# Kernel optimization log

Hardware: AMD Instinct MI355X
Metric: run time of the kernel (lower is better)

Reference implementation:

```python
import jax, jax.numpy as jnp
import numpy as np

B, L, H, IN, NL = 8, 32768, 96, 1, 2


def _init(k, shape):
    # PyTorch LSTM/Linear default: U(-1/sqrt(H), 1/sqrt(H))
    return jax.random.uniform(k, shape, jnp.float32, -1.0, 1.0) / np.float32(np.sqrt(H))


def setup_inputs() -> dict:
    key = jax.random.key(0)
    ks = jax.random.split(key, 16)
    W_ih_0 = _init(ks[0], (4 * H, IN))
    W_hh_0 = _init(ks[1], (4 * H, H))
    b_ih_0 = _init(ks[2], (4 * H,))
    b_hh_0 = _init(ks[3], (4 * H,))
    W_ih_1 = _init(ks[4], (4 * H, H))
    W_hh_1 = _init(ks[5], (4 * H, H))
    b_ih_1 = _init(ks[6], (4 * H,))
    b_hh_1 = _init(ks[7], (4 * H,))
    # custom _L.reset_parameters: input-gate bias -=2, forget-gate bias +=2 on BOTH biases
    off = jnp.concatenate([jnp.full((H,), -2.0), jnp.full((H,), 2.0), jnp.zeros((2 * H,))]).astype(jnp.float32)
    b_0 = b_ih_0 + b_hh_0 + 2.0 * off  # combined bias per layer (they only ever add)
    b_1 = b_ih_1 + b_hh_1 + 2.0 * off
    head_w = _init(ks[8], (1, H))
    head_b = _init(ks[9], (1,))
    h0 = jnp.zeros((NL, H), jnp.float32)  # nn.Parameter initial hidden
    c0 = jnp.zeros((NL, H), jnp.float32)  # nn.Parameter initial cell
    x = 0.5 * jax.random.normal(ks[10], (B, L), jnp.float32)
    return {"x": x, "W_ih_0": W_ih_0, "W_hh_0": W_hh_0, "b_0": b_0,
            "W_ih_1": W_ih_1, "W_hh_1": W_hh_1, "b_1": b_1,
            "h0": h0, "c0": c0, "head_w": head_w, "head_b": head_b}


def _lstm_layer(x, W_ih, W_hh, b, h0, c0):
    # x: (B, L, D_in) -> hidden outputs (B, L, H). PyTorch gate order: i, f, g, o.
    Bn = x.shape[0]
    Hd = W_hh.shape[1]
    xp = jnp.einsum('bld,gd->blg', x, W_ih) + b  # (B, L, 4H), precompute input proj

    def step(carry, xt):
        h, c = carry
        gates = xt + h @ W_hh.T
        i, f, g, o = jnp.split(gates, 4, axis=-1)
        c = jax.nn.sigmoid(f) * c + jax.nn.sigmoid(i) * jnp.tanh(g)
        h = jax.nn.sigmoid(o) * jnp.tanh(c)
        return (h, c), h

    h0b = jnp.broadcast_to(h0, (Bn, Hd))
    c0b = jnp.broadcast_to(c0, (Bn, Hd))
    _, hs = jax.lax.scan(step, (h0b, c0b), jnp.swapaxes(xp, 0, 1))  # (L, B, H)
    return jnp.swapaxes(hs, 0, 1)


def reference(x, W_ih_0, W_hh_0, b_0, W_ih_1, W_hh_1, b_1, h0, c0, head_w, head_b):
    feats = x[:, :, None]  # (B, L, 1)
    feats = _lstm_layer(feats, W_ih_0, W_hh_0, b_0, h0[0], c0[0])
    feats = _lstm_layer(feats, W_ih_1, W_hh_1, b_1, h0[1], c0[1])
    # head: Linear(H, 1) then squeeze last dim -> (B, L)
    return jnp.einsum('blh,oh->bl', feats, head_w) + head_b[0]
```

## Files before the change

### kernel.cpp

```cpp
#include <hip/hip_runtime.h>

#define HDIM 96
#define G4   384
#define LSEQ 32768
#define BATCH 8
#define TCH   1024
#define NCH   (LSEQ / TCH)

#define L2E  1.4426950408889634f
#define SNEG (-L2E)
#define SPOS (2.0f * L2E)

__device__ __forceinline__ float tanh_(float x) {
    return fmaf(-2.f, __builtin_amdgcn_rcpf(1.f + __builtin_amdgcn_exp2f(SPOS * x)), 1.f);
}

#define DPPSTEP(v, CTRL) { \
    int t_ = __builtin_amdgcn_update_dpp(0, __float_as_int(v), CTRL, 0xF, 0xF, true); \
    v += __int_as_float(t_); }
#define DPPADDV(u, v, CTRL) { \
    int t_ = __builtin_amdgcn_update_dpp(0, __float_as_int(v), CTRL, 0xF, 0xF, true); \
    u += __int_as_float(t_); }

#define QBCAST(DST, SRCI, CTRL) \
    float DST = __int_as_float(__builtin_amdgcn_update_dpp(0, (SRCI), (CTRL), 0xF, 0xF, true));

#define BARL() asm volatile("s_waitcnt lgkmcnt(0)\n\ts_barrier" ::: "memory")

#define PIN4x3(A,B,C) asm volatile("" : \
  "+v"(A.x),"+v"(A.y),"+v"(A.z),"+v"(A.w), \
  "+v"(B.x),"+v"(B.y),"+v"(B.z),"+v"(B.w), \
  "+v"(C.x),"+v"(C.y),"+v"(C.z),"+v"(C.w));

#define SC4(V, S) { V.x *= (S); V.y *= (S); V.z *= (S); V.w *= (S); }

#define WLOADPIN(W) \
    const float4* pI = reinterpret_cast<const float4*>((W) + (size_t)e        * HDIM + 12*s); \
    const float4* pF = reinterpret_cast<const float4*>((W) + (size_t)(96 + e) * HDIM + 12*s); \
    const float4* pG = reinterpret_cast<const float4*>((W) + (size_t)(192+ e) * HDIM + 12*s); \
    const float4* pO = reinterpret_cast<const float4*>((W) + (size_t)(288+ e) * HDIM + 12*s); \
    float4 wI0=pI[0], wI1=pI[1], wI2=pI[2]; \
    float4 wF0=pF[0], wF1=pF[1], wF2=pF[2]; \
    float4 wG0=pG[0], wG1=pG[1], wG2=pG[2]; \
    float4 wO0=pO[0], wO1=pO[1], wO2=pO[2]; \
    SC4(wI0,SNEG) SC4(wI1,SNEG) SC4(wI2,SNEG) \
    SC4(wF0,SNEG) SC4(wF1,SNEG) SC4(wF2,SNEG) \
    SC4(wG0,SPOS) SC4(wG1,SPOS) SC4(wG2,SPOS) \
    SC4(wO0,SNEG) SC4(wO1,SNEG) SC4(wO2,SNEG) \
    PIN4x3(wI0,wI1,wI2) PIN4x3(wF0,wF1,wF2) PIN4x3(wG0,wG1,wG2) PIN4x3(wO0,wO1,wO2)

#define MVK(n, hv) \
  gi=fmaf(wI##n.x,hv.x,gi); gi=fmaf(wI##n.y,hv.y,gi); gi=fmaf(wI##n.z,hv.z,gi); gi=fmaf(wI##n.w,hv.w,gi); \
  gf=fmaf(wF##n.x,hv.x,gf); gf=fmaf(wF##n.y,hv.y,gf); gf=fmaf(wF##n.z,hv.z,gf); gf=fmaf(wF##n.w,hv.w,gf); \
  gg=fmaf(wG##n.x,hv.x,gg); gg=fmaf(wG##n.y,hv.y,gg); gg=fmaf(wG##n.z,hv.z,gg); gg=fmaf(wG##n.w,hv.w,gg); \
  go=fmaf(wO##n.x,hv.x,go); go=fmaf(wO##n.y,hv.y,go); go=fmaf(wO##n.z,hv.z,go); go=fmaf(wO##n.w,hv.w,go);

#define GATES_TAIL(DEST_STORE) \
    float uA = (tsel & 1) ? gf : gi,  vA = (tsel & 1) ? gi : gf; \
    float uB = (tsel & 1) ? go : gg,  vB = (tsel & 1) ? gg : go; \
    DPPADDV(uA, vA, 0xB1)  DPPADDV(uB, vB, 0xB1) \
    float uC = (tsel & 2) ? uB : uA,  vC = (tsel & 2) ? uA : uB; \
    DPPADDV(uC, vC, 0x4E) \
    DPPSTEP(uC, 0x141) \
    float E_ = __builtin_amdgcn_exp2f(uC); \
    float r_ = __builtin_amdgcn_rcpf(1.f + E_); \
    int ai = __float_as_int(fmaf(mC, r_, aC)); \
    QBCAST(si, ai, 0x00) \
    QBCAST(sf, ai, 0x55) \
    QBCAST(tg, ai, 0xAA) \
    QBCAST(so, ai, 0xFF) \
    cU = fmaf(sf, cU, si * tg); \
    float hN = so * tanh_(cU); \
    DEST_STORE

#define STEP0(RO, XT) { \
    const float4* hp = reinterpret_cast<const float4*>(hs + (RO) + 12 * s); \
    float4 hv0 = hp[0], hv1 = hp[1], hv2 = hp[2]; \
    float gi = fmaf(wiI, (XT), bbI); \
    float gf = fmaf(wiF, (XT), bbF); \
    float gg = fmaf(wiG, (XT), bbG); \
    float go = fmaf(wiO, (XT), bbO); \
    MVK(0, hv0) MVK(1, hv1) MVK(2, hv2) \
    GATES_TAIL( \
      if (w0l) { hs[((RO) ^ HDIM) + e] = hN; *hobp = hN; } \
      hobp += HDIM; ) }

#define STEP2(RO, XPV) { \
    const float4* hp = reinterpret_cast<const float4*>(hs + (RO) + 12 * s); \
    float4 hv0 = hp[0], hv1 = hp[1], hv2 = hp[2]; \
    float gi = (XPV).x, gf = (XPV).y, gg = (XPV).z, go = (XPV).w; \
    MVK(0, hv0) MVK(1, hv1) MVK(2, hv2) \
    GATES_TAIL( \
      if (w0l) { hs[((RO) ^ HDIM) + e] = hN; *h1p = hN; } \
      h1p += HDIM; ) }

#define WAIT_GE(PTR, VAL) \
    while (__hip_atomic_load((PTR), __ATOMIC_ACQUIRE, __HIP_MEMORY_SCOPE_AGENT) < (VAL)) \
        __builtin_amdgcn_s_sleep(2);

#define SIGNAL(PTR, VAL) \
    __hip_atomic_store((PTR), (VAL), __ATOMIC_RELEASE, __HIP_MEMORY_SCOPE_AGENT);

__global__ void init_flags(int* flags) {
    if (threadIdx.x < 64) flags[threadIdx.x] = 0;
}

__global__ void __launch_bounds__(768)
__attribute__((amdgpu_waves_per_eu(3, 3)))
lstm_pipe(const float* __restrict__ x,
          const float* __restrict__ Wih0, const float* __restrict__ Whh0, const float* __restrict__ b0v,
          const float* __restrict__ Wih1, const float* __restrict__ Whh1, const float* __restrict__ b1v,
          const float* __restrict__ h0v,  const float* __restrict__ c0v,
          const float* __restrict__ headw,const float* __restrict__ headb,
          float* __restrict__ h0buf, float* __restrict__ xpbuf, float* __restrict__ h1buf,
          int* flags, float* __restrict__ out)
{
    const int tid  = threadIdx.x;
    const int lane = tid & 63;
    const int e    = tid >> 3;
    const int s    = tid & 7;
    const bool w0l = ((lane & 7) == 0);

    int* flag0 = flags;
    int* flag1 = flags + 8;
    int* flag2 = flags + 16;
    int* flag3 = flags + 24;

    __shared__ __align__(16) float hs[2 * HDIM];
    __shared__ __align__(16) float h_sh[32 * HDIM];
    __shared__ float ph_sh[2 * G4];

    const int role = blockIdx.x >> 3;
    const int bidx = blockIdx.x & 7;

    const int tsel = (s & 3) ^ ((s & 4) ? 3 : 0);
    const float mC = (tsel == 2) ? -2.f : 1.f;
    const float aC = (tsel == 2) ?  1.f : 0.f;

    if (role == 0) {
        WLOADPIN(Whh0)
        const float wiI = Wih0[e]      * (SNEG * 0.125f);
        const float wiF = Wih0[96 + e] * (SNEG * 0.125f);
        const float wiG = Wih0[192+ e] * (SPOS * 0.125f);
        const float wiO = Wih0[288+ e] * (SNEG * 0.125f);
        const float bbI = b0v[e]       * (SNEG * 0.125f);
        const float bbF = b0v[96 + e]  * (SNEG * 0.125f);
        const float bbG = b0v[192+ e]  * (SPOS * 0.125f);
        const float bbO = b0v[288+ e]  * (SNEG * 0.125f);

        float cU = c0v[e];
        if (w0l) hs[e] = h0v[e];
        __syncthreads();

        const float* xb  = x + (size_t)bidx * LSEQ;
        float*       hobp = h0buf + (size_t)bidx * LSEQ * HDIM + e;

        float4 xA = *reinterpret_cast<const float4*>(xb);

#pragma unroll 1
        for (int gI = 0; gI < LSEQ / 8; ++gI) {
            float4 xB = *reinterpret_cast<const float4*>(xb + gI * 8 + 4);
            STEP0(0,    xA.x) BARL();
            STEP0(HDIM, xA.y) BARL();
            STEP0(0,    xA.z) BARL();
            STEP0(HDIM, xA.w) BARL();
            float4 xAn = *reinterpret_cast<const float4*>(
                xb + (((gI + 1) * 8 < LSEQ) ? (gI + 1) * 8 : LSEQ - 8));
            STEP0(0,    xB.x) BARL();
            STEP0(HDIM, xB.y) BARL();
            STEP0(0,    xB.z) BARL();
            STEP0(HDIM, xB.w)
            xA = xAn;
            if (((gI + 1) & 127) == 0) {
                __threadfence();
                __syncthreads();
                if (tid == 0) SIGNAL(&flag0[bidx], (gI + 1) >> 7)
            } else {
                BARL();
            }
        }
    } else if (role == 1) {
        const bool halfx = (tid >= G4);
        const int  g     = halfx ? tid - G4 : tid;
        const int  dstoff = (g % 96) * 4 + (g / 96);
        const float gsc  = (((g / 96) == 2) ? SPOS : SNEG) * 0.125f;
        const float4* Wxp = reinterpret_cast<const float4*>(Wih1 + (size_t)g * HDIM + (halfx ? 48 : 0));
        const float xbias = halfx ? 0.f : b1v[g] * gsc;

        float4 q0=Wxp[0],q1=Wxp[1],q2=Wxp[2],q3=Wxp[3],q4=Wxp[4],q5=Wxp[5],
               q6=Wxp[6],q7=Wxp[7],q8=Wxp[8],q9=Wxp[9],q10=Wxp[10],q11=Wxp[11];
        SC4(q0,gsc) SC4(q1,gsc) SC4(q2,gsc)  SC4(q3,gsc) SC4(q4,gsc)  SC4(q5,gsc)
        SC4(q6,gsc) SC4(q7,gsc) SC4(q8,gsc)  SC4(q9,gsc) SC4(q10,gsc) SC4(q11,gsc)
        PIN4x3(q0,q1,q2) PIN4x3(q3,q4,q5) PIN4x3(q6,q7,q8) PIN4x3(q9,q10,q11)

        const float* hsrcB = h0buf + (size_t)bidx * LSEQ * HDIM;

#pragma unroll 1
        for (int k = 0; k < NCH; ++k) {
            if (tid == 0) {
                WAIT_GE(&flag0[bidx], k + 1)
                if (k >= 2) WAIT_GE(&flag2[bidx], k - 1)
            }
            __syncthreads();
            __threadfence();

            const float* hsrc = hsrcB + (size_t)k * TCH * HDIM;
            float* xpd = xpbuf + ((size_t)bidx * 2 + (k & 1)) * TCH * G4;

#pragma unroll 1
            for (int t0 = 0; t0 < TCH; t0 += 32) {
                reinterpret_cast<float4*>(h_sh)[tid] =
                    reinterpret_cast<const float4*>(hsrc + (size_t)t0 * HDIM)[tid];
                BARL();
#pragma unroll 1
                for (int tt = 0; tt < 32; ++tt) {
                    const float4* h4 = reinterpret_cast<const float4*>(
                        h_sh + tt * HDIM + (halfx ? 48 : 0));
                    float a0 = xbias, a1 = 0.f, a2 = 0.f, a3 = 0.f;
                    float4 hv;
                    hv=h4[0];  a0=fmaf(q0.x, hv.x,a0); a1=fmaf(q0.y, hv.y,a1); a2=fmaf(q0.z, hv.z,a2); a3=fmaf(q0.w, hv.w,a3);
                    hv=h4[1];  a0=fmaf(q1.x, hv.x,a0); a1=fmaf(q1.y, hv.y,a1); a2=fmaf(q1.z, hv.z,a2); a3=fmaf(q1.w, hv.w,a3);
                    hv=h4[2];  a0=fmaf(q2.x, hv.x,a0); a1=fmaf(q2.y, hv.y,a1); a2=fmaf(q2.z, hv.z,a2); a3=fmaf(q2.w, hv.w,a3);
                    hv=h4[3];  a0=fmaf(q3.x, hv.x,a0); a1=fmaf(q3.y, hv.y,a1); a2=fmaf(q3.z, hv.z,a2); a3=fmaf(q3.w, hv.w,a3);
                    hv=h4[4];  a0=fmaf(q4.x, hv.x,a0); a1=fmaf(q4.y, hv.y,a1); a2=fmaf(q4.z, hv.z,a2); a3=fmaf(q4.w, hv.w,a3);
                    hv=h4[5];  a0=fmaf(q5.x, hv.x,a0); a1=fmaf(q5.y, hv.y,a1); a2=fmaf(q5.z, hv.z,a2); a3=fmaf(q5.w, hv.w,a3);
                    hv=h4[6];  a0=fmaf(q6.x, hv.x,a0); a1=fmaf(q6.y, hv.y,a1); a2=fmaf(q6.z, hv.z,a2); a3=fmaf(q6.w, hv.w,a3);
                    hv=h4[7];  a0=fmaf(q7.x, hv.x,a0); a1=fmaf(q7.y, hv.y,a1); a2=fmaf(q7.z, hv.z,a2); a3=fmaf(q7.w, hv.w,a3);
                    hv=h4[8];  a0=fmaf(q8.x, hv.x,a0); a1=fmaf(q8.y, hv.y,a1); a2=fmaf(q8.z, hv.z,a2); a3=fmaf(q8.w, hv.w,a3);
                    hv=h4[9];  a0=fmaf(q9.x, hv.x,a0); a1=fmaf(q9.y, hv.y,a1); a2=fmaf(q9.z, hv.z,a2); a3=fmaf(q9.w, hv.w,a3);
                    hv=h4[10]; a0=fmaf(q10.x,hv.x,a0); a1=fmaf(q10.y,hv.y,a1); a2=fmaf(q10.z,hv.z,a2); a3=fmaf(q10.w,hv.w,a3);
                    hv=h4[11]; a0=fmaf(q11.x,hv.x,a0); a1=fmaf(q11.y,hv.y,a1); a2=fmaf(q11.z,hv.z,a2); a3=fmaf(q11.w,hv.w,a3);
                    float part = (a0 + a1) + (a2 + a3);
                    float* ph2 = ph_sh + ((tt & 1) ? G4 : 0);
                    if (halfx) ph2[g] = part;
                    BARL();
                    if (!halfx) xpd[(size_t)(t0 + tt) * G4 + dstoff] = part + ph2[g];
                }
                BARL();
            }
            __threadfence();
            __syncthreads();
            if (tid == 0) SIGNAL(&flag1[bidx], k + 1)
        }
    } else if (role == 2) {
        WLOADPIN(Whh1)

        float cU = c0v[HDIM + e];
        if (w0l) hs[e] = h0v[HDIM + e];
        __syncthreads();

#pragma unroll 1
        for (int k = 0; k < NCH; ++k) {
            if (tid == 0) {
                WAIT_GE(&flag1[bidx], k + 1)
                if (k >= 2) WAIT_GE(&flag3[bidx], k - 1)
            }
            __syncthreads();
            __threadfence();

            const float4* xq  = reinterpret_cast<const float4*>(
                xpbuf + ((size_t)bidx * 2 + (k & 1)) * TCH * G4) + e;
            float* h1p = h1buf + ((size_t)bidx * 2 + (k & 1)) * TCH * HDIM + e;

            float4 a0 = xq[0], a1 = xq[HDIM], a2 = xq[2 * HDIM], a3 = xq[3 * HDIM];

#pragma unroll 1
            for (int gI = 0; gI < TCH / 8; ++gI) {
                const float4* xg = xq + (size_t)gI * 8 * HDIM;
                float4 b0_, b1_, b2_, b3_;
                STEP2(0,    a0) b0_ = xg[4 * HDIM]; BARL();
                STEP2(HDIM, a1) b1_ = xg[5 * HDIM]; BARL();
                STEP2(0,    a2) b2_ = xg[6 * HDIM]; BARL();
                STEP2(HDIM, a3) b3_ = xg[7 * HDIM]; BARL();
                const float4* xn = xq + (size_t)((gI + 1 < TCH / 8) ? (gI + 1) * 8 : TCH - 8) * HDIM;
                STEP2(0,    b0_) a0 = xn[0];        BARL();
                STEP2(HDIM, b1_) a1 = xn[HDIM];     BARL();
                STEP2(0,    b2_) a2 = xn[2 * HDIM]; BARL();
                STEP2(HDIM, b3_) a3 = xn[3 * HDIM]; BARL();
            }
            __threadfence();
            __syncthreads();
            if (tid == 0) SIGNAL(&flag2[bidx], k + 1)
        }
    } else {
        const float hb = headb[0];
        float4 wv[24];
#pragma unroll
        for (int j = 0; j < 24; ++j) wv[j] = reinterpret_cast<const float4*>(headw)[j];

#pragma unroll 1
        for (int k = 0; k < NCH; ++k) {
            if (tid == 0) WAIT_GE(&flag2[bidx], k + 1)
            __syncthreads();
            __threadfence();

            const float* h1c = h1buf + ((size_t)bidx * 2 + (k & 1)) * TCH * HDIM;
            for (int t = tid; t < TCH; t += 768) {
                const float4* hp = reinterpret_cast<const float4*>(h1c + (size_t)t * HDIM);
                float s2 = 0.f;
#pragma unroll
                for (int j = 0; j < 24; ++j) {
                    float4 a = hp[j], b = wv[j];
                    s2 = fmaf(a.x, b.x, s2); s2 = fmaf(a.y, b.y, s2);
                    s2 = fmaf(a.z, b.z, s2); s2 = fmaf(a.w, b.w, s2);
                }
                out[(size_t)bidx * LSEQ + (size_t)k * TCH + t] = s2 + hb;
            }
            __threadfence();
            __syncthreads();
            if (tid == 0) SIGNAL(&flag3[bidx], k + 1)
        }
    }
}

extern "C" void kernel_launch(void* const* d_in, const int* in_sizes, int n_in,
                              void* d_out, int out_size, void* d_ws, size_t ws_size,
                              hipStream_t stream)
{
    const float* x     = (const float*)d_in[0];
    const float* Wih0  = (const float*)d_in[1];
    const float* Whh0  = (const float*)d_in[2];
    const float* b0    = (const float*)d_in[3];
    const float* Wih1  = (const float*)d_in[4];
    const float* Whh1  = (const float*)d_in[5];
    const float* b1    = (const float*)d_in[6];
    const float* h0    = (const float*)d_in[7];
    const float* c0    = (const float*)d_in[8];
    const float* headw = (const float*)d_in[9];
    const float* headb = (const float*)d_in[10];
    float* out = (float*)d_out;

    char* ws = (char*)d_ws;
    const size_t h0bytes = (size_t)BATCH * LSEQ * HDIM * sizeof(float);
    const size_t xpbytes = (size_t)BATCH * 2 * TCH * G4 * sizeof(float);
    const size_t h1bytes = (size_t)BATCH * 2 * TCH * HDIM * sizeof(float);

    float* h0buf = (float*)ws;
    float* xpbuf = (float*)(ws + h0bytes);
    float* h1buf = (float*)(ws + h0bytes + xpbytes);
    int*   flags = (int*)  (ws + h0bytes + xpbytes + h1bytes);

    init_flags<<<1, 64, 0, stream>>>(flags);
    lstm_pipe<<<32, 768, 0, stream>>>(x, Wih0, Whh0, b0, Wih1, Whh1, b1,
                                      h0, c0, headw, headb,
                                      h0buf, xpbuf, h1buf, flags, out);
}
```

Baseline: 14.18 ms.

## Interleave two batch sequences per block to hide recurrent step latency

Each block now runs two independent batch sequences side by side: both recurrent roles interleave steps for two batches between barriers, and the projection and head roles loop over both batches. The grid drops from 32 to 16 blocks. The goal is to spread barrier and DPP/transcendental latency across two independent dependency chains, giving more instruction-level parallelism per barrier. The cost is twice the serial work per block, plus more register pressure and a doubled projection load on each projection block.

```diff
diff --git a/kernel.cpp b/kernel.cpp
--- a/kernel.cpp
+++ b/kernel.cpp
@@ -55,7 +55,7 @@
   gg=fmaf(wG##n.x,hv.x,gg); gg=fmaf(wG##n.y,hv.y,gg); gg=fmaf(wG##n.z,hv.z,gg); gg=fmaf(wG##n.w,hv.w,gg); \
   go=fmaf(wO##n.x,hv.x,go); go=fmaf(wO##n.y,hv.y,go); go=fmaf(wO##n.z,hv.z,go); go=fmaf(wO##n.w,hv.w,go);
 
-#define GATES_TAIL(DEST_STORE) \
+#define GATES_TAILX(CUV, DEST_STORE) \
     float uA = (tsel & 1) ? gf : gi,  vA = (tsel & 1) ? gi : gf; \
     float uB = (tsel & 1) ? go : gg,  vB = (tsel & 1) ? gg : go; \
     DPPADDV(uA, vA, 0xB1)  DPPADDV(uB, vB, 0xB1) \
@@ -69,30 +69,30 @@
     QBCAST(sf, ai, 0x55) \
     QBCAST(tg, ai, 0xAA) \
     QBCAST(so, ai, 0xFF) \
-    cU = fmaf(sf, cU, si * tg); \
-    float hN = so * tanh_(cU); \
+    CUV = fmaf(sf, CUV, si * tg); \
+    float hN = so * tanh_(CUV); \
     DEST_STORE
 
-#define STEP0(RO, XT) { \
-    const float4* hp = reinterpret_cast<const float4*>(hs + (RO) + 12 * s); \
+#define STEP0X(BASE, OFF, XT, CUV, HOBP) { \
+    const float4* hp = reinterpret_cast<const float4*>(hs2 + (BASE) + (OFF) + 12 * s); \
     float4 hv0 = hp[0], hv1 = hp[1], hv2 = hp[2]; \
     float gi = fmaf(wiI, (XT), bbI); \
     float gf = fmaf(wiF, (XT), bbF); \
     float gg = fmaf(wiG, (XT), bbG); \
     float go = fmaf(wiO, (XT), bbO); \
     MVK(0, hv0) MVK(1, hv1) MVK(2, hv2) \
-    GATES_TAIL( \
-      if (w0l) { hs[((RO) ^ HDIM) + e] = hN; *hobp = hN; } \
-      hobp += HDIM; ) }
-
-#define STEP2(RO, XPV) { \
-    const float4* hp = reinterpret_cast<const float4*>(hs + (RO) + 12 * s); \
+    GATES_TAILX(CUV, \
+      if (w0l) { hs2[(BASE) + ((OFF) ^ HDIM) + e] = hN; *(HOBP) = hN; } \
+      (HOBP) += HDIM; ) }
+
+#define STEP2X(BASE, OFF, XPV, CUV, H1P) { \
+    const float4* hp = reinterpret_cast<const float4*>(hs2 + (BASE) + (OFF) + 12 * s); \
     float4 hv0 = hp[0], hv1 = hp[1], hv2 = hp[2]; \
     float gi = (XPV).x, gf = (XPV).y, gg = (XPV).z, go = (XPV).w; \
     MVK(0, hv0) MVK(1, hv1) MVK(2, hv2) \
-    GATES_TAIL( \
-      if (w0l) { hs[((RO) ^ HDIM) + e] = hN; *h1p = hN; } \
-      h1p += HDIM; ) }
+    GATES_TAILX(CUV, \
+      if (w0l) { hs2[(BASE) + ((OFF) ^ HDIM) + e] = hN; *(H1P) = hN; } \
+      (H1P) += HDIM; ) }
 
 #define WAIT_GE(PTR, VAL) \
     while (__hip_atomic_load((PTR), __ATOMIC_ACQUIRE, __HIP_MEMORY_SCOPE_AGENT) < (VAL)) \
@@ -126,12 +126,14 @@
     int* flag2 = flags + 16;
     int* flag3 = flags + 24;
 
-    __shared__ __align__(16) float hs[2 * HDIM];
+    __shared__ __align__(16) float hs2[2 * 2 * HDIM];
     __shared__ __align__(16) float h_sh[32 * HDIM];
     __shared__ float ph_sh[2 * G4];
 
-    const int role = blockIdx.x >> 3;
-    const int bidx = blockIdx.x & 7;
+    const int role = blockIdx.x >> 2;
+    const int pr   = blockIdx.x & 3;
+    const int bA   = 2 * pr;
+    const int bB   = 2 * pr + 1;
 
     const int tsel = (s & 3) ^ ((s & 4) ? 3 : 0);
     const float mC = (tsel == 2) ? -2.f : 1.f;
@@ -148,33 +150,38 @@
         const float bbG = b0v[192+ e]  * (SPOS * 0.125f);
         const float bbO = b0v[288+ e]  * (SNEG * 0.125f);
 
-        float cU = c0v[e];
-        if (w0l) hs[e] = h0v[e];
+        float cUA = c0v[e], cUB = c0v[e];
+        if (w0l) { hs2[e] = h0v[e]; hs2[192 + e] = h0v[e]; }
         __syncthreads();
 
-        const float* xb  = x + (size_t)bidx * LSEQ;
-        float*       hobp = h0buf + (size_t)bidx * LSEQ * HDIM + e;
-
-        float4 xA = *reinterpret_cast<const float4*>(xb);
+        const float* xbA = x + (size_t)bA * LSEQ;
+        const float* xbB = x + (size_t)bB * LSEQ;
+        float* hobpA = h0buf + (size_t)bA * LSEQ * HDIM + e;
+        float* hobpB = h0buf + (size_t)bB * LSEQ * HDIM + e;
+
+        float4 xAA = *reinterpret_cast<const float4*>(xbA);
+        float4 xAB = *reinterpret_cast<const float4*>(xbB);
 
 #pragma unroll 1
         for (int gI = 0; gI < LSEQ / 8; ++gI) {
-            float4 xB = *reinterpret_cast<const float4*>(xb + gI * 8 + 4);
-            STEP0(0,    xA.x) BARL();
-            STEP0(HDIM, xA.y) BARL();
-            STEP0(0,    xA.z) BARL();
-            STEP0(HDIM, xA.w) BARL();
-            float4 xAn = *reinterpret_cast<const float4*>(
-                xb + (((gI + 1) * 8 < LSEQ) ? (gI + 1) * 8 : LSEQ - 8));
-            STEP0(0,    xB.x) BARL();
-            STEP0(HDIM, xB.y) BARL();
-            STEP0(0,    xB.z) BARL();
-            STEP0(HDIM, xB.w)
-            xA = xAn;
+            float4 xBA = *reinterpret_cast<const float4*>(xbA + gI * 8 + 4);
+            float4 xBB = *reinterpret_cast<const float4*>(xbB + gI * 8 + 4);
+            STEP0X(0,  0,    xAA.x, cUA, hobpA) STEP0X(192, 0,    xAB.x, cUB, hobpB) BARL();
+            STEP0X(0,  HDIM, xAA.y, cUA, hobpA) STEP0X(192, HDIM, xAB.y, cUB, hobpB) BARL();
+            STEP0X(0,  0,    xAA.z, cUA, hobpA) STEP0X(192, 0,    xAB.z, cUB, hobpB) BARL();
+            STEP0X(0,  HDIM, xAA.w, cUA, hobpA) STEP0X(192, HDIM, xAB.w, cUB, hobpB) BARL();
+            const int nOff = ((gI + 1) * 8 < LSEQ) ? (gI + 1) * 8 : LSEQ - 8;
+            float4 xAnA = *reinterpret_cast<const float4*>(xbA + nOff);
+            float4 xAnB = *reinterpret_cast<const float4*>(xbB + nOff);
+            STEP0X(0,  0,    xBA.x, cUA, hobpA) STEP0X(192, 0,    xBB.x, cUB, hobpB) BARL();
+            STEP0X(0,  HDIM, xBA.y, cUA, hobpA) STEP0X(192, HDIM, xBB.y, cUB, hobpB) BARL();
+            STEP0X(0,  0,    xBA.z, cUA, hobpA) STEP0X(192, 0,    xBB.z, cUB, hobpB) BARL();
+            STEP0X(0,  HDIM, xBA.w, cUA, hobpA) STEP0X(192, HDIM, xBB.w, cUB, hobpB)
+            xAA = xAnA; xAB = xAnB;
             if (((gI + 1) & 127) == 0) {
                 __threadfence();
                 __syncthreads();
-                if (tid == 0) SIGNAL(&flag0[bidx], (gI + 1) >> 7)
+                if (tid == 0) SIGNAL(&flag0[pr], (gI + 1) >> 7)
             } else {
                 BARL();
             }
@@ -193,94 +200,111 @@
         SC4(q6,gsc) SC4(q7,gsc) SC4(q8,gsc)  SC4(q9,gsc) SC4(q10,gsc) SC4(q11,gsc)
         PIN4x3(q0,q1,q2) PIN4x3(q3,q4,q5) PIN4x3(q6,q7,q8) PIN4x3(q9,q10,q11)
 
-        const float* hsrcB = h0buf + (size_t)bidx * LSEQ * HDIM;
-
 #pragma unroll 1
         for (int k = 0; k < NCH; ++k) {
             if (tid == 0) {
-                WAIT_GE(&flag0[bidx], k + 1)
-                if (k >= 2) WAIT_GE(&flag2[bidx], k - 1)
-            }
-            __syncthreads();
-            __threadfence();
-
-            const float* hsrc = hsrcB + (size_t)k * TCH * HDIM;
-            float* xpd = xpbuf + ((size_t)bidx * 2 + (k & 1)) * TCH * G4;
-
-#pragma unroll 1
-            for (int t0 = 0; t0 < TCH; t0 += 32) {
-                reinterpret_cast<float4*>(h_sh)[tid] =
-                    reinterpret_cast<const float4*>(hsrc + (size_t)t0 * HDIM)[tid];
-                BARL();
-#pragma unroll 1
-                for (int tt = 0; tt < 32; ++tt) {
-                    const float4* h4 = reinterpret_cast<const float4*>(
-                        h_sh + tt * HDIM + (halfx ? 48 : 0));
-                    float a0 = xbias, a1 = 0.f, a2 = 0.f, a3 = 0.f;
-                    float4 hv;
-                    hv=h4[0];  a0=fmaf(q0.x, hv.x,a0); a1=fmaf(q0.y, hv.y,a1); a2=fmaf(q0.z, hv.z,a2); a3=fmaf(q0.w, hv.w,a3);
-                    hv=h4[1];  a0=fmaf(q1.x, hv.x,a0); a1=fmaf(q1.y, hv.y,a1); a2=fmaf(q1.z, hv.z,a2); a3=fmaf(q1.w, hv.w,a3);
-                    hv=h4[2];  a0=fmaf(q2.x, hv.x,a0); a1=fmaf(q2.y, hv.y,a1); a2=fmaf(q2.z, hv.z,a2); a3=fmaf(q2.w, hv.w,a3);
-                    hv=h4[3];  a0=fmaf(q3.x, hv.x,a0); a1=fmaf(q3.y, hv.y,a1); a2=fmaf(q3.z, hv.z,a2); a3=fmaf(q3.w, hv.w,a3);
-                    hv=h4[4];  a0=fmaf(q4.x, hv.x,a0); a1=fmaf(q4.y, hv.y,a1); a2=fmaf(q4.z, hv.z,a2); a3=fmaf(q4.w, hv.w,a3);
-                    hv=h4[5];  a0=fmaf(q5.x, hv.x,a0); a1=fmaf(q5.y, hv.y,a1); a2=fmaf(q5.z, hv.z,a2); a3=fmaf(q5.w, hv.w,a3);
-                    hv=h4[6];  a0=fmaf(q6.x, hv.x,a0); a1=fmaf(q6.y, hv.y,a1); a2=fmaf(q6.z, hv.z,a2); a3=fmaf(q6.w, hv.w,a3);
-                    hv=h4[7];  a0=fmaf(q7.x, hv.x,a0); a1=fmaf(q7.y, hv.y,a1); a2=fmaf(q7.z, hv.z,a2); a3=fmaf(q7.w, hv.w,a3);
-                    hv=h4[8];  a0=fmaf(q8.x, hv.x,a0); a1=fmaf(q8.y, hv.y,a1); a2=fmaf(q8.z, hv.z,a2); a3=fmaf(q8.w, hv.w,a3);
-                    hv=h4[9];  a0=fmaf(q9.x, hv.x,a0); a1=fmaf(q9.y, hv.y,a1); a2=fmaf(q9.z, hv.z,a2); a3=fmaf(q9.w, hv.w,a3);
-                    hv=h4[10]; a0=fmaf(q10.x,hv.x,a0); a1=fmaf(q10.y,hv.y,a1); a2=fmaf(q10.z,hv.z,a2); a3=fmaf(q10.w,hv.w,a3);
-                    hv=h4[11]; a0=fmaf(q11.x,hv.x,a0); a1=fmaf(q11.y,hv.y,a1); a2=fmaf(q11.z,hv.z,a2); a3=fmaf(q11.w,hv.w,a3);
-                    float part = (a0 + a1) + (a2 + a3);
-                    float* ph2 = ph_sh + ((tt & 1) ? G4 : 0);
-                    if (halfx) ph2[g] = part;
+                WAIT_GE(&flag0[pr], k + 1)
+                if (k >= 2) WAIT_GE(&flag2[pr], k - 1)
+            }
+            __syncthreads();
+            __threadfence();
+
+#pragma unroll 1
+            for (int bb = 0; bb < 2; ++bb) {
+                const int b = 2 * pr + bb;
+                const float* hsrc = h0buf + (size_t)b * LSEQ * HDIM + (size_t)k * TCH * HDIM;
+                float* xpd = xpbuf + ((size_t)b * 2 + (k & 1)) * TCH * G4;
+
+#pragma unroll 1
+                for (int t0 = 0; t0 < TCH; t0 += 32) {
+                    reinterpret_cast<float4*>(h_sh)[tid] =
+                        reinterpret_cast<const float4*>(hsrc + (size_t)t0 * HDIM)[tid];
                     BARL();
-                    if (!halfx) xpd[(size_t)(t0 + tt) * G4 + dstoff] = part + ph2[g];
+#pragma unroll 1
+                    for (int tt = 0; tt < 32; ++tt) {
+                        const float4* h4 = reinterpret_cast<const float4*>(
+                            h_sh + tt * HDIM + (halfx ? 48 : 0));
+                        float a0 = xbias, a1 = 0.f, a2 = 0.f, a3 = 0.f;
+                        float4 hv;
+                        hv=h4[0];  a0=fmaf(q0.x, hv.x,a0); a1=fmaf(q0.y, hv.y,a1); a2=fmaf(q0.z, hv.z,a2); a3=fmaf(q0.w, hv.w,a3);
+                        hv=h4[1];  a0=fmaf(q1.x, hv.x,a0); a1=fmaf(q1.y, hv.y,a1); a2=fmaf(q1.z, hv.z,a2); a3=fmaf(q1.w, hv.w,a3);
+                        hv=h4[2];  a0=fmaf(q2.x, hv.x,a0); a1=fmaf(q2.y, hv.y,a1); a2=fmaf(q2.z, hv.z,a2); a3=fmaf(q2.w, hv.w,a3);
+                        hv=h4[3];  a0=fmaf(q3.x, hv.x,a0); a1=fmaf(q3.y, hv.y,a1); a2=fmaf(q3.z, hv.z,a2); a3=fmaf(q3.w, hv.w,a3);
+                        hv=h4[4];  a0=fmaf(q4.x, hv.x,a0); a1=fmaf(q4.y, hv.y,a1); a2=fmaf(q4.z, hv.z,a2); a3=fmaf(q4.w, hv.w,a3);
+                        hv=h4[5];  a0=fmaf(q5.x, hv.x,a0); a1=fmaf(q5.y, hv.y,a1); a2=fmaf(q5.z, hv.z,a2); a3=fmaf(q5.w, hv.w,a3);
+                        hv=h4[6];  a0=fmaf(q6.x, hv.x,a0); a1=fmaf(q6.y, hv.y,a1); a2=fmaf(q6.z, hv.z,a2); a3=fmaf(q6.w, hv.w,a3);
+                        hv=h4[7];  a0=fmaf(q7.x, hv.x,a0); a1=fmaf(q7.y, hv.y,a1); a2=fmaf(q7.z, hv.z,a2); a3=fmaf(q7.w, hv.w,a3);
+                        hv=h4[8];  a0=fmaf(q8.x, hv.x,a0); a1=fmaf(q8.y, hv.y,a1); a2=fmaf(q8.z, hv.z,a2); a3=fmaf(q8.w, hv.w,a3);
+                        hv=h4[9];  a0=fmaf(q9.x, hv.x,a0); a1=fmaf(q9.y, hv.y,a1); a2=fmaf(q9.z, hv.z,a2); a3=fmaf(q9.w, hv.w,a3);
+                        hv=h4[10]; a0=fmaf(q10.x,hv.x,a0); a1=fmaf(q10.y,hv.y,a1); a2=fmaf(q10.z,hv.z,a2); a3=fmaf(q10.w,hv.w,a3);
+                        hv=h4[11]; a0=fmaf(q11.x,hv.x,a0); a1=fmaf(q11.y,hv.y,a1); a2=fmaf(q11.z,hv.z,a2); a3=fmaf(q11.w,hv.w,a3);
+                        float part = (a0 + a1) + (a2 + a3);
+                        float* ph2 = ph_sh + ((tt & 1) ? G4 : 0);
+                        if (halfx) ph2[g] = part;
+                        BARL();
+                        if (!halfx) xpd[(size_t)(t0 + tt) * G4 + dstoff] = part + ph2[g];
+                    }
+                    BARL();
                 }
-                BARL();
-            }
-            __threadfence();
-            __syncthreads();
-            if (tid == 0) SIGNAL(&flag1[bidx], k + 1)
+            }
+            __threadfence();
+            __syncthreads();
+            if (tid == 0) SIGNAL(&flag1[pr], k + 1)
         }
     } else if (role == 2) {
         WLOADPIN(Whh1)
 
-        float cU = c0v[HDIM + e];
-        if (w0l) hs[e] = h0v[HDIM + e];
+        float cUA = c0v[HDIM + e], cUB = c0v[HDIM + e];
+        if (w0l) { hs2[e] = h0v[HDIM + e]; hs2[192 + e] = h0v[HDIM + e]; }
         __syncthreads();
 
 #pragma unroll 1
         for (int k = 0; k < NCH; ++k) {
             if (tid == 0) {
-                WAIT_GE(&flag1[bidx], k + 1)
-                if (k >= 2) WAIT_GE(&flag3[bidx], k - 1)
-            }
-            __syncthreads();
-            __threadfence();
-
-            const float4* xq  = reinterpret_cast<const float4*>(
-                xpbuf + ((size_t)bidx * 2 + (k & 1)) * TCH * G4) + e;
-            float* h1p = h1buf + ((size_t)bidx * 2 + (k & 1)) * TCH * HDIM + e;
-
-            float4 a0 = xq[0], a1 = xq[HDIM], a2 = xq[2 * HDIM], a3 = xq[3 * HDIM];
+                WAIT_GE(&flag1[pr], k + 1)
+                if (k >= 2) WAIT_GE(&flag3[pr], k - 1)
+            }
+            __syncthreads();
+            __threadfence();
+
+            const float4* xqA = reinterpret_cast<const float4*>(
+                xpbuf + ((size_t)bA * 2 + (k & 1)) * TCH * G4) + e;
+            const float4* xqB = reinterpret_cast<const float4*>(
+                xpbuf + ((size_t)bB * 2 + (k & 1)) * TCH * G4) + e;
+            float* h1pA = h1buf + ((size_t)bA * 2 + (k & 1)) * TCH * HDIM + e;
+            float* h1pB = h1buf + ((size_t)bB * 2 + (k & 1)) * TCH * HDIM + e;
+
+            float4 aA0 = xqA[0], aA1 = xqA[HDIM], aA2 = xqA[2 * HDIM], aA3 = xqA[3 * HDIM];
+            float4 aB0 = xqB[0], aB1 = xqB[HDIM], aB2 = xqB[2 * HDIM], aB3 = xqB[3 * HDIM];
 
 #pragma unroll 1
             for (int gI = 0; gI < TCH / 8; ++gI) {
-                const float4* xg = xq + (size_t)gI * 8 * HDIM;
-                float4 b0_, b1_, b2_, b3_;
-                STEP2(0,    a0) b0_ = xg[4 * HDIM]; BARL();
-                STEP2(HDIM, a1) b1_ = xg[5 * HDIM]; BARL();
-                STEP2(0,    a2) b2_ = xg[6 * HDIM]; BARL();
-                STEP2(HDIM, a3) b3_ = xg[7 * HDIM]; BARL();
-                const float4* xn = xq + (size_t)((gI + 1 < TCH / 8) ? (gI + 1) * 8 : TCH - 8) * HDIM;
-                STEP2(0,    b0_) a0 = xn[0];        BARL();
-                STEP2(HDIM, b1_) a1 = xn[HDIM];     BARL();
-                STEP2(0,    b2_) a2 = xn[2 * HDIM]; BARL();
-                STEP2(HDIM, b3_) a3 = xn[3 * HDIM]; BARL();
-            }
-            __threadfence();
-            __syncthreads();
-            if (tid == 0) SIGNAL(&flag2[bidx], k + 1)
+                const float4* xgA = xqA + (size_t)gI * 8 * HDIM;
+                const float4* xgB = xqB + (size_t)gI * 8 * HDIM;
+                float4 bA0_, bA1_, bA2_, bA3_, bB0_, bB1_, bB2_, bB3_;
+                STEP2X(0,  0,    aA0, cUA, h1pA) STEP2X(192, 0,    aB0, cUB, h1pB)
+                bA0_ = xgA[4 * HDIM]; bB0_ = xgB[4 * HDIM]; BARL();
+                STEP2X(0,  HDIM, aA1, cUA, h1pA) STEP2X(192, HDIM, aB1, cUB, h1pB)
+                bA1_ = xgA[5 * HDIM]; bB1_ = xgB[5 * HDIM]; BARL();
+                STEP2X(0,  0,    aA2, cUA, h1pA) STEP2X(192, 0,    aB2, cUB, h1pB)
+                bA2_ = xgA[6 * HDIM]; bB2_ = xgB[6 * HDIM]; BARL();
+                STEP2X(0,  HDIM, aA3, cUA, h1pA) STEP2X(192, HDIM, aB3, cUB, h1pB)
+                bA3_ = xgA[7 * HDIM]; bB3_ = xgB[7 * HDIM]; BARL();
+                const size_t nO = (size_t)((gI + 1 < TCH / 8) ? (gI + 1) * 8 : TCH - 8) * HDIM;
+                const float4* xnA = xqA + nO;
+                const float4* xnB = xqB + nO;
+                STEP2X(0,  0,    bA0_, cUA, h1pA) STEP2X(192, 0,    bB0_, cUB, h1pB)
+                aA0 = xnA[0];        aB0 = xnB[0];        BARL();
+                STEP2X(0,  HDIM, bA1_, cUA, h1pA) STEP2X(192, HDIM, bB1_, cUB, h1pB)
+                aA1 = xnA[HDIM];     aB1 = xnB[HDIM];     BARL();
+                STEP2X(0,  0,    bA2_, cUA, h1pA) STEP2X(192, 0,    bB2_, cUB, h1pB)
+                aA2 = xnA[2 * HDIM]; aB2 = xnB[2 * HDIM]; BARL();
+                STEP2X(0,  HDIM, bA3_, cUA, h1pA) STEP2X(192, HDIM, bB3_, cUB, h1pB)
+                aA3 = xnA[3 * HDIM]; aB3 = xnB[3 * HDIM]; BARL();
+            }
+            __threadfence();
+            __syncthreads();
+            if (tid == 0) SIGNAL(&flag2[pr], k + 1)
         }
     } else {
         const float hb = headb[0];
@@ -290,25 +314,29 @@
 
 #pragma unroll 1
         for (int k = 0; k < NCH; ++k) {
-            if (tid == 0) WAIT_GE(&flag2[bidx], k + 1)
-            __syncthreads();
-            __threadfence();
-
-            const float* h1c = h1buf + ((size_t)bidx * 2 + (k & 1)) * TCH * HDIM;
-            for (int t = tid; t < TCH; t += 768) {
-                const float4* hp = reinterpret_cast<const float4*>(h1c + (size_t)t * HDIM);
-                float s2 = 0.f;
+            if (tid == 0) WAIT_GE(&flag2[pr], k + 1)
+            __syncthreads();
+            __threadfence();
+
+#pragma unroll 1
+            for (int bb = 0; bb < 2; ++bb) {
+                const int b = 2 * pr + bb;
+                const float* h1c = h1buf + ((size_t)b * 2 + (k & 1)) * TCH * HDIM;
+                for (int t = tid; t < TCH; t += 768) {
+                    const float4* hp = reinterpret_cast<const float4*>(h1c + (size_t)t * HDIM);
+                    float s2 = 0.f;
 #pragma unroll
-                for (int j = 0; j < 24; ++j) {
-                    float4 a = hp[j], b = wv[j];
-                    s2 = fmaf(a.x, b.x, s2); s2 = fmaf(a.y, b.y, s2);
-                    s2 = fmaf(a.z, b.z, s2); s2 = fmaf(a.w, b.w, s2);
+                    for (int j = 0; j < 24; ++j) {
+                        float4 a = hp[j], bwv = wv[j];
+                        s2 = fmaf(a.x, bwv.x, s2); s2 = fmaf(a.y, bwv.y, s2);
+                        s2 = fmaf(a.z, bwv.z, s2); s2 = fmaf(a.w, bwv.w, s2);
+                    }
+                    out[(size_t)b * LSEQ + (size_t)k * TCH + t] = s2 + hb;
                 }
-                out[(size_t)bidx * LSEQ + (size_t)k * TCH + t] = s2 + hb;
-            }
-            __threadfence();
-            __syncthreads();
-            if (tid == 0) SIGNAL(&flag3[bidx], k + 1)
+            }
+            __threadfence();
+            __syncthreads();
+            if (tid == 0) SIGNAL(&flag3[pr], k + 1)
         }
     }
 }
@@ -341,7 +369,7 @@
     int*   flags = (int*)  (ws + h0bytes + xpbytes + h1bytes);
 
     init_flags<<<1, 64, 0, stream>>>(flags);
-    lstm_pipe<<<32, 768, 0, stream>>>(x, Wih0, Whh0, b0, Wih1, Whh1, b1,
+    lstm_pipe<<<16, 768, 0, stream>>>(x, Wih0, Whh0, b0, Wih1, Whh1, b1,
                                       h0, c0, headw, headb,
                                       h0buf, xpbuf, h1buf, flags, out);
 }
```

Result: slower. 27.46 ms (+93.6%).
